# Kernel tuning notes

Hardware: AMD Instinct MI355X
Metric: run time of the kernel (lower is better)

## Reference

```python
import jax, jax.numpy as jnp
import numpy as np

D_MODEL = 512
D_STATE = 64
D_CONV = 4
EXPAND = 2
D_INNER = D_MODEL * EXPAND  # 1024
DT_RANK = 32  # ceil(512/16)
BATCH = 2
SEQLEN = 1024


def setup_inputs() -> dict:
    key = jax.random.key(0)
    ks = jax.random.split(key, 8)
    s = 0.02
    x = jax.random.normal(ks[0], (BATCH, SEQLEN, D_MODEL), dtype=jnp.float32)
    W_in = jax.random.normal(ks[1], (2 * D_INNER, D_MODEL), dtype=jnp.float32) * s
    conv_w = jax.random.normal(ks[2], (D_INNER, 1, D_CONV), dtype=jnp.float32) * s
    conv_b = jnp.zeros((D_INNER,), dtype=jnp.float32)
    W_x = jax.random.normal(ks[3], (DT_RANK + 2 * D_STATE, D_INNER), dtype=jnp.float32) * s
    W_dt = jax.random.normal(ks[4], (D_INNER, DT_RANK), dtype=jnp.float32) * s
    b_dt = jax.random.uniform(ks[5], (D_INNER,), dtype=jnp.float32) * (DT_RANK ** -0.5)
    A_log = jnp.log(jnp.arange(1, D_STATE + 1, dtype=jnp.float32))
    D_param = jnp.ones((D_INNER,), dtype=jnp.float32)
    W_out = jax.random.normal(ks[6], (D_MODEL, D_INNER), dtype=jnp.float32) * s
    return {"x": x, "W_in": W_in, "conv_w": conv_w, "conv_b": conv_b,
            "W_x": W_x, "W_dt": W_dt, "b_dt": b_dt, "A_log": A_log,
            "D_param": D_param, "W_out": W_out}


def _mamba_fwd(x, W_in, conv_w, conv_b, W_x, W_dt, b_dt, A_log, D_param, W_out):
    Bb, L, _ = x.shape
    # input projection -> [B,L,2*d_inner], split into SSM branch and gate
    xz = x @ W_in.T
    xs, z = jnp.split(xz, 2, axis=-1)
    # causal depthwise conv1d (torch pads d_conv-1 both sides then slices [:L])
    xc = jnp.transpose(xs, (0, 2, 1))  # [B, d_inner, L]
    xc = jax.lax.conv_general_dilated(
        xc, conv_w, window_strides=(1,), padding=[(D_CONV - 1, 0)],
        dimension_numbers=('NCH', 'OIH', 'NCH'), feature_group_count=D_INNER)
    xc = xc + conv_b[None, :, None]
    xs = jax.nn.silu(jnp.transpose(xc, (0, 2, 1)))  # [B,L,d_inner]
    # selective parameters
    dbc = xs @ W_x.T  # [B,L,dt_rank+2N]
    dt, Bm, Cm = jnp.split(dbc, [DT_RANK, DT_RANK + D_STATE], axis=-1)
    delta = jax.nn.softplus(dt @ W_dt.T + b_dt)  # [B,L,d_inner]
    A = -jnp.exp(A_log)  # [N]
    dA = jnp.exp(delta[..., None] * A)                 # [B,L,D,N]
    dBx = (delta * xs)[..., None] * Bm[:, :, None, :]  # [B,L,D,N]

    def step(h, inp):
        dA_t, dBx_t, C_t = inp
        h = dA_t * h + dBx_t                 # [B,D,N]
        y_t = jnp.einsum('bdn,bn->bd', h, C_t)
        return h, y_t

    h0 = jnp.zeros((Bb, D_INNER, D_STATE), dtype=x.dtype)
    _, ys = jax.lax.scan(step, h0, (jnp.swapaxes(dA, 0, 1),
                                    jnp.swapaxes(dBx, 0, 1),
                                    jnp.swapaxes(Cm, 0, 1)))
    y = jnp.swapaxes(ys, 0, 1) + D_param * xs  # skip term
    y = y * jax.nn.silu(z)                     # gate
    return y @ W_out.T


def reference(x, W_in, conv_w, conv_b, W_x, W_dt, b_dt, A_log, D_param, W_out):
    return _mamba_fwd(x, W_in, conv_w, conv_b, W_x, W_dt, b_dt, A_log, D_param, W_out)
```

## Files before the change

### kernel.cpp

```cpp
#include <hip/hip_runtime.h>
#include <hip/hip_bf16.h>
#include <math.h>

#define D_STATE 64
#define D_INNER 1024
#define DT_RANK 32
#define BATCH 2
#define SEQLEN 1024
#define MTOT (BATCH * SEQLEN)
#define NCC 64
#define CHT 16

typedef __attribute__((ext_vector_type(8))) short bf16x8;
typedef __attribute__((ext_vector_type(4))) float f32x4;

__device__ __forceinline__ float silu_f(float x) { return x / (1.f + __expf(-x)); }

__global__ __launch_bounds__(256) void cast_bf16_k(
    const float* __restrict__ in, __hip_bfloat16* __restrict__ out, int n)
{
    int i = (blockIdx.x * 256 + threadIdx.x) * 4;
    if (i >= n) return;
    float4 v = *(const float4*)(in + i);
    __hip_bfloat16 o[4] = {__float2bfloat16(v.x), __float2bfloat16(v.y),
                           __float2bfloat16(v.z), __float2bfloat16(v.w)};
    *(short4*)(out + i) = *(const short4*)o;
}

__global__ __launch_bounds__(256) void cast3_k(
    const float* __restrict__ p0, __hip_bfloat16* __restrict__ o0,
    const float* __restrict__ p1, __hip_bfloat16* __restrict__ o1,
    const float* __restrict__ p2, __hip_bfloat16* __restrict__ o2)
{
    int b = blockIdx.x;
    const float* in; __hip_bfloat16* out; int base;
    if (b < 1024)      { in = p0; out = o0; base = b; }
    else if (b < 2048) { in = p1; out = o1; base = b - 1024; }
    else               { in = p2; out = o2; base = b - 2048; }
    int i = (base * 256 + threadIdx.x) * 4;
    float4 v = *(const float4*)(in + i);
    __hip_bfloat16 o[4] = {__float2bfloat16(v.x), __float2bfloat16(v.y),
                           __float2bfloat16(v.z), __float2bfloat16(v.w)};
    *(short4*)(out + i) = *(const short4*)o;
}

template<int BM, int BN>
__global__ __launch_bounds__((BM / 64) * (BN / 64) * 64) void gemm_bf16(
    const __hip_bfloat16* __restrict__ A, const __hip_bfloat16* __restrict__ Bt,
    float* __restrict__ C, int M, int N, int K)
{
    constexpr int NW = (BM / 64) * (BN / 64);
    constexpr int NT = NW * 64;
    constexpr int NWN = BN / 64;
    __shared__ __align__(16) short As[BM][40];
    __shared__ __align__(16) short Bs[BN][40];
    const int tid = threadIdx.x;
    const int m0 = blockIdx.y * BM, n0 = blockIdx.x * BN;
    const int wid = tid >> 6, lane = tid & 63;
    const int wm = wid / NWN, wn = wid % NWN;
    const int lrow = lane & 15, lkg = (lane >> 4) * 8;

    f32x4 acc[4][4] = {};

    for (int k0 = 0; k0 < K; k0 += 32) {
        for (int i = tid * 8; i < BM * 32; i += NT * 8) {
            int r = i >> 5, c = i & 31;
            *(bf16x8*)&As[r][c] =
                *(const bf16x8*)(A + (size_t)(m0 + r) * K + k0 + c);
        }
        for (int i = tid * 8; i < BN * 32; i += NT * 8) {
            int r = i >> 5, c = i & 31;
            bf16x8 v = {};
            if (n0 + r < N)
                v = *(const bf16x8*)(Bt + (size_t)(n0 + r) * K + k0 + c);
            *(bf16x8*)&Bs[r][c] = v;
        }
        __syncthreads();
        bf16x8 af[4], bfr[4];
        #pragma unroll
        for (int mi = 0; mi < 4; ++mi)
            af[mi] = *(const bf16x8*)&As[wm * 64 + mi * 16 + lrow][lkg];
        #pragma unroll
        for (int ni = 0; ni < 4; ++ni)
            bfr[ni] = *(const bf16x8*)&Bs[wn * 64 + ni * 16 + lrow][lkg];
        #pragma unroll
        for (int mi = 0; mi < 4; ++mi)
            #pragma unroll
            for (int ni = 0; ni < 4; ++ni)
                acc[mi][ni] = __builtin_amdgcn_mfma_f32_16x16x32_bf16(
                    af[mi], bfr[ni], acc[mi][ni], 0, 0, 0);
        __syncthreads();
    }

    const int rbase = (lane >> 4) * 4;
    #pragma unroll
    for (int mi = 0; mi < 4; ++mi) {
        #pragma unroll
        for (int ni = 0; ni < 4; ++ni) {
            int col = n0 + wn * 64 + ni * 16 + lrow;
            if (col < N) {
                #pragma unroll
                for (int r = 0; r < 4; ++r) {
                    int row = m0 + wm * 64 + mi * 16 + rbase + r;
                    C[(size_t)row * N + col] = acc[mi][ni][r];
                }
            }
        }
    }
}

template<int MF>
__global__ __launch_bounds__(256) void gemm_bf16_w(
    const __hip_bfloat16* __restrict__ A, const __hip_bfloat16* __restrict__ Bt,
    float* __restrict__ C, int M, int N, int K)
{
    const int tid = threadIdx.x;
    const int wid = tid >> 6, lane = tid & 63;
    const int m0 = blockIdx.y * (64 * MF) + wid * (16 * MF);
    const int n0 = blockIdx.x * 64;
    const int lrow = lane & 15, kg8 = (lane >> 4) * 8;

    f32x4 acc[MF][4] = {};
    #pragma unroll 2
    for (int k0 = 0; k0 < K; k0 += 32) {
        bf16x8 af[MF];
        #pragma unroll
        for (int mi = 0; mi < MF; ++mi)
            af[mi] = *(const bf16x8*)(A + (size_t)(m0 + mi * 16 + lrow) * K + k0 + kg8);
        #pragma unroll
        for (int ni = 0; ni < 4; ++ni) {
            int r = n0 + ni * 16 + lrow;
            bf16x8 bv = {};
            if (r < N) bv = *(const bf16x8*)(Bt + (size_t)r * K + k0 + kg8);
            #pragma unroll
            for (int mi = 0; mi < MF; ++mi)
                acc[mi][ni] = __builtin_amdgcn_mfma_f32_16x16x32_bf16(
                    af[mi], bv, acc[mi][ni], 0, 0, 0);
        }
    }
    const int rbase = (lane >> 4) * 4;
    #pragma unroll
    for (int mi = 0; mi < MF; ++mi) {
        #pragma unroll
        for (int ni = 0; ni < 4; ++ni) {
            int col = n0 + ni * 16 + lrow;
            if (col < N) {
                #pragma unroll
                for (int r = 0; r < 4; ++r)
                    C[(size_t)(m0 + mi * 16 + rbase + r) * N + col] = acc[mi][ni][r];
            }
        }
    }
}

__global__ __launch_bounds__(256) void conv_silu_k(
    const float* __restrict__ xz, const float* __restrict__ cw,
    const float* __restrict__ cb, float* __restrict__ xs,
    __hip_bfloat16* __restrict__ xs_bf)
{
    int e = blockIdx.x * 256 + threadIdx.x;
    int d = (e & 255) * 4;
    int ml = e >> 8;
    int l = ml & (SEQLEN - 1);
    int b = ml >> 10;
    float4 c0 = *(const float4*)(cw + (d + 0) * 4);
    float4 c1 = *(const float4*)(cw + (d + 1) * 4);
    float4 c2 = *(const float4*)(cw + (d + 2) * 4);
    float4 c3 = *(const float4*)(cw + (d + 3) * 4);
    float cwk[4][4] = {{c0.x, c0.y, c0.z, c0.w}, {c1.x, c1.y, c1.z, c1.w},
                       {c2.x, c2.y, c2.z, c2.w}, {c3.x, c3.y, c3.z, c3.w}};
    float4 acc = *(const float4*)(cb + d);
    #pragma unroll
    for (int k = 0; k < 4; ++k) {
        int t = l - 3 + k;
        if (t >= 0) {
            float4 xv = *(const float4*)(xz + (size_t)(b * SEQLEN + t) * 2048 + d);
            acc.x = fmaf(xv.x, cwk[0][k], acc.x);
            acc.y = fmaf(xv.y, cwk[1][k], acc.y);
            acc.z = fmaf(xv.z, cwk[2][k], acc.z);
            acc.w = fmaf(xv.w, cwk[3][k], acc.w);
        }
    }
    float4 v = {silu_f(acc.x), silu_f(acc.y), silu_f(acc.z), silu_f(acc.w)};
    size_t o = (size_t)ml * D_INNER + d;
    *(float4*)(xs + o) = v;
    __hip_bfloat16 ob[4] = {__float2bfloat16(v.x), __float2bfloat16(v.y),
                            __float2bfloat16(v.z), __float2bfloat16(v.w)};
    *(short4*)(xs_bf + o) = *(const short4*)ob;
}

__global__ __launch_bounds__(256) void delta_softplus_k(
    const float* __restrict__ dbc, const float* __restrict__ Wdt,
    const float* __restrict__ bdt, float* __restrict__ delta)
{
    const int tid = threadIdx.x;
    const int mg = blockIdx.x * 8;
    #pragma unroll
    for (int j = 0; j < 4; ++j) {
        const int n = tid + j * 256;
        float w[32];
        const float4* wr = (const float4*)(Wdt + (size_t)n * 32);
        #pragma unroll
        for (int q = 0; q < 8; ++q) {
            float4 v = wr[q];
            w[q * 4 + 0] = v.x; w[q * 4 + 1] = v.y;
            w[q * 4 + 2] = v.z; w[q * 4 + 3] = v.w;
        }
        const float bias = bdt[n];
        #pragma unroll
        for (int m = 0; m < 8; ++m) {
            const float* dt = dbc + (size_t)(mg + m) * 160;
            float acc = bias;
            #pragma unroll
            for (int k = 0; k < 32; ++k) acc = fmaf(dt[k], w[k], acc);
            float sp = (acc > 20.f) ? acc : log1pf(__expf(acc));
            delta[(size_t)(mg + m) * D_INNER + n] = sp;
        }
    }
}


#define SLC_A(H, BB, CC) H = fmaf(a, H, dx * BB); p = fmaf(H, CC, p); a *= E;
#define SL_BODY(H, SD, DD, B0, B1, B2, B3, C0, C1, C2, C3, YL) { \
    SD += DD.x; \
    float E = __expf(-DD.x); \
    float a = __expf(DD.x * wn0); \
    float dx = DD.y; float p = 0.f; \
    SLC_A(H[0], B0.x, C0.x) SLC_A(H[1], B0.y, C0.y) SLC_A(H[2], B0.z, C0.z) SLC_A(H[3], B0.w, C0.w) \
    SLC_A(H[4], B1.x, C1.x) SLC_A(H[5], B1.y, C1.y) SLC_A(H[6], B1.z, C1.z) SLC_A(H[7], B1.w, C1.w) \
    SLC_A(H[8], B2.x, C2.x) SLC_A(H[9], B2.y, C2.y) SLC_A(H[10], B2.z, C2.z) SLC_A(H[11], B2.w, C2.w) \
    SLC_A(H[12], B3.x, C3.x) SLC_A(H[13], B3.y, C3.y) SLC_A(H[14], B3.z, C3.z) SLC_A(H[15], B3.w, C3.w) \
    YL = p; }

__global__ __launch_bounds__(256, 2) void scan_local_k(
    const float* __restrict__ delta, const float* __restrict__ xs,
    const float* __restrict__ dbc, const float* __restrict__ Alog,
    float* __restrict__ S, float* __restrict__ sumd, float* __restrict__ xzbuf)
{
    __shared__ float2 ddxs[2][CHT][64];
    __shared__ float yl[2][4][CHT][64];
    const int tid = threadIdx.x;
    const int pair = blockIdx.x & 31;
    const int dblk = (blockIdx.x >> 5) & 15;
    const int b = blockIdx.x >> 9;
    const int d0 = dblk * 64;
    const int cA = pair, cB = pair + 32;
    const int mA = b * SEQLEN + cA * CHT;
    const int mB = b * SEQLEN + cB * CHT;

    #pragma unroll
    for (int i = tid; i < 2 * CHT * 16; i += 256) {
        int s = i >= CHT * 16;
        int j = i - s * CHT * 16;
        int t = j >> 4, dq = (j & 15) * 4;
        int mbase = s ? mB : mA;
        size_t idx = (size_t)(mbase + t) * D_INNER + d0 + dq;
        float4 dl = *(const float4*)(delta + idx);
        float4 xv = *(const float4*)(xs + idx);
        float4 w1 = {dl.x, dl.x * xv.x, dl.y, dl.y * xv.y};
        float4 w2 = {dl.z, dl.z * xv.z, dl.w, dl.w * xv.w};
        *(float4*)&ddxs[s][t][dq] = w1;
        *(float4*)&ddxs[s][t][dq + 2] = w2;
    }
    __syncthreads();

    const int w = tid >> 6, lane = tid & 63;
    const int nbu = __builtin_amdgcn_readfirstlane(w * 16);
    const float* __restrict__ BpA = dbc + (size_t)mA * 160 + 32 + nbu;
    const float* __restrict__ BpB = dbc + (size_t)mB * 160 + 32 + nbu;
    const float wn0 = -__expf(Alog[nbu]);
    float ha[16], hb[16];
    #pragma unroll
    for (int i = 0; i < 16; ++i) { ha[i] = 0.f; hb[i] = 0.f; }
    float sdA = 0.f, sdB = 0.f;

    #pragma unroll 2
    for (int t = 0; t < CHT; ++t) {
        float2 dA = ddxs[0][t][lane];
        float2 dB = ddxs[1][t][lane];
        float4 A0 = *(const float4*)(BpA + t * 160);
        float4 A1 = *(const float4*)(BpA + t * 160 + 4);
        float4 A2 = *(const float4*)(BpA + t * 160 + 8);
        float4 A3 = *(const float4*)(BpA + t * 160 + 12);
        float4 AC0 = *(const float4*)(BpA + t * 160 + 64);
        float4 AC1 = *(const float4*)(BpA + t * 160 + 68);
        float4 AC2 = *(const float4*)(BpA + t * 160 + 72);
        float4 AC3 = *(const float4*)(BpA + t * 160 + 76);
        float4 B0 = *(const float4*)(BpB + t * 160);
        float4 B1 = *(const float4*)(BpB + t * 160 + 4);
        float4 B2 = *(const float4*)(BpB + t * 160 + 8);
        float4 B3 = *(const float4*)(BpB + t * 160 + 12);
        float4 BC0 = *(const float4*)(BpB + t * 160 + 64);
        float4 BC1 = *(const float4*)(BpB + t * 160 + 68);
        float4 BC2 = *(const float4*)(BpB + t * 160 + 72);
        float4 BC3 = *(const float4*)(BpB + t * 160 + 76);
        SL_BODY(ha, sdA, dA, A0, A1, A2, A3, AC0, AC1, AC2, AC3, yl[0][w][t][lane])
        SL_BODY(hb, sdB, dB, B0, B1, B2, B3, BC0, BC1, BC2, BC3, yl[1][w][t][lane])
    }

    size_t baseA = ((size_t)(b * NCC + cA) * 16 + dblk) * 4096;
    size_t baseB = ((size_t)(b * NCC + cB) * 16 + dblk) * 4096;
    #pragma unroll
    for (int i = 0; i < 16; ++i) {
        S[baseA + (size_t)(nbu + i) * 64 + lane] = ha[i];
        S[baseB + (size_t)(nbu + i) * 64 + lane] = hb[i];
    }
    if (w == 0) {
        sumd[(size_t)(b * NCC + cA) * D_INNER + d0 + lane] = sdA;
        sumd[(size_t)(b * NCC + cB) * D_INNER + d0 + lane] = sdB;
    }
    __syncthreads();

    #pragma unroll
    for (int i = tid; i < 2 * CHT * 16; i += 256) {
        int s = i >= CHT * 16;
        int j = i - s * CHT * 16;
        int t = j >> 4, dq = (j & 15) * 4;
        int m = (s ? mB : mA) + t;
        float4 y0 = *(const float4*)&yl[s][0][t][dq];
        float4 y1 = *(const float4*)&yl[s][1][t][dq];
        float4 y2 = *(const float4*)&yl[s][2][t][dq];
        float4 y3 = *(const float4*)&yl[s][3][t][dq];
        float4 yv = {y0.x + y1.x + y2.x + y3.x, y0.y + y1.y + y2.y + y3.y,
                     y0.z + y1.z + y2.z + y3.z, y0.w + y1.w + y2.w + y3.w};
        *(float4*)(xzbuf + (size_t)m * 2048 + d0 + dq) = yv;
    }
}

__global__ __launch_bounds__(256) void scan_mid_k(
    float* SH, const float* __restrict__ sumd, const float* __restrict__ Alog)
{
    int g = blockIdx.x * 256 + threadIdx.x;
    int d = g & 63;
    int n = (g >> 6) & 63;
    int dblk = (g >> 12) & 15;
    int b = g >> 16;
    float An = -__expf(Alog[n]);
    float h = 0.f;
    #pragma unroll 4
    for (int c = 0; c < NCC; ++c) {
        size_t idx = ((size_t)(b * NCC + c) * 16 + dblk) * 4096 + (size_t)n * 64 + d;
        float s = SH[idx];
        float P = __expf(An * sumd[(size_t)(b * NCC + c) * D_INNER + dblk * 64 + d]);
        SH[idx] = h;
        h = fmaf(P, h, s);
    }
}

#define CR_A(H, CC) p = fmaf(ai * H, CC, p); ai *= E;
#define CR_BODY(H, CD, C0, C1, C2, C3, YL) { \
    float a = __expf(CD * wn0); \
    float E = __expf(-CD); \
    float ai = a; float p = 0.f; \
    CR_A(H[0], C0.x) CR_A(H[1], C0.y) CR_A(H[2], C0.z) CR_A(H[3], C0.w) \
    CR_A(H[4], C1.x) CR_A(H[5], C1.y) CR_A(H[6], C1.z) CR_A(H[7], C1.w) \
    CR_A(H[8], C2.x) CR_A(H[9], C2.y) CR_A(H[10], C2.z) CR_A(H[11], C2.w) \
    CR_A(H[12], C3.x) CR_A(H[13], C3.y) CR_A(H[14], C3.z) CR_A(H[15], C3.w) \
    YL = p; }

__global__ __launch_bounds__(256, 2) void scan_corr_k(
    const float* __restrict__ delta, const float* __restrict__ xs,
    const float* __restrict__ dbc, const float* __restrict__ Alog,
    const float* __restrict__ H, const float* __restrict__ xz,
    const float* __restrict__ Dp, __hip_bfloat16* __restrict__ y)
{
    __shared__ float cum[2][CHT][64];
    __shared__ float yl[2][4][CHT][64];
    const int tid = threadIdx.x;
    const int pair = blockIdx.x & 31;
    const int dblk = (blockIdx.x >> 5) & 15;
    const int b = blockIdx.x >> 9;
    const int d0 = dblk * 64;
    const int cA = pair, cB = pair + 32;
    const int mA = b * SEQLEN + cA * CHT;
    const int mB = b * SEQLEN + cB * CHT;

    #pragma unroll
    for (int i = tid; i < 2 * CHT * 16; i += 256) {
        int s = i >= CHT * 16;
        int j = i - s * CHT * 16;
        int t = j >> 4, dq = (j & 15) * 4;
        int mbase = s ? mB : mA;
        *(float4*)&cum[s][t][dq] =
            *(const float4*)(delta + (size_t)(mbase + t) * D_INNER + d0 + dq);
    }
    __syncthreads();
    if (tid < 128) {
        int s = tid >> 6, d = tid & 63;
        float run = 0.f;
        #pragma unroll
        for (int t = 0; t < CHT; ++t) {
            run += cum[s][t][d];
            cum[s][t][d] = run;
        }
    }
    __syncthreads();

    const int w = tid >> 6, lane = tid & 63;
    const int nbu = __builtin_amdgcn_readfirstlane(w * 16);
    const float* __restrict__ CpA = dbc + (size_t)mA * 160 + 96 + nbu;
    const float* __restrict__ CpB = dbc + (size_t)mB * 160 + 96 + nbu;
    const float wn0 = -__expf(Alog[nbu]);
    size_t baseA = ((size_t)(b * NCC + cA) * 16 + dblk) * 4096;
    size_t baseB = ((size_t)(b * NCC + cB) * 16 + dblk) * 4096;
    float ha[16], hb[16];
    #pragma unroll
    for (int i = 0; i < 16; ++i) {
        ha[i] = H[baseA + (size_t)(nbu + i) * 64 + lane];
        hb[i] = H[baseB + (size_t)(nbu + i) * 64 + lane];
    }

    #pragma unroll 4
    for (int t = 0; t < CHT; ++t) {
        float cdA = cum[0][t][lane];
        float cdB = cum[1][t][lane];
        float4 CA0 = *(const float4*)(CpA + t * 160);
        float4 CA1 = *(const float4*)(CpA + t * 160 + 4);
        float4 CA2 = *(const float4*)(CpA + t * 160 + 8);
        float4 CA3 = *(const float4*)(CpA + t * 160 + 12);
        float4 CB0 = *(const float4*)(CpB + t * 160);
        float4 CB1 = *(const float4*)(CpB + t * 160 + 4);
        float4 CB2 = *(const float4*)(CpB + t * 160 + 8);
        float4 CB3 = *(const float4*)(CpB + t * 160 + 12);
        CR_BODY(ha, cdA, CA0, CA1, CA2, CA3, yl[0][w][t][lane])
        CR_BODY(hb, cdB, CB0, CB1, CB2, CB3, yl[1][w][t][lane])
    }
    __syncthreads();

    #pragma unroll
    for (int i = tid; i < 2 * CHT * 16; i += 256) {
        int s = i >= CHT * 16;
        int j = i - s * CHT * 16;
        int t = j >> 4, dq = (j & 15) * 4;
        int m = (s ? mB : mA) + t;
        int dg = d0 + dq;
        float4 y0 = *(const float4*)&yl[s][0][t][dq];
        float4 y1 = *(const float4*)&yl[s][1][t][dq];
        float4 y2 = *(const float4*)&yl[s][2][t][dq];
        float4 y3 = *(const float4*)&yl[s][3][t][dq];
        float4 yloc = *(const float4*)(xz + (size_t)m * 2048 + dg);
        float4 yv = {yloc.x + y0.x + y1.x + y2.x + y3.x,
                     yloc.y + y0.y + y1.y + y2.y + y3.y,
                     yloc.z + y0.z + y1.z + y2.z + y3.z,
                     yloc.w + y0.w + y1.w + y2.w + y3.w};
        float4 xv = *(const float4*)(xs + (size_t)m * D_INNER + dg);
        float4 zv = *(const float4*)(xz + (size_t)m * 2048 + D_INNER + dg);
        float4 Dv = *(const float4*)(Dp + dg);
        __hip_bfloat16 o[4] = {
            __float2bfloat16((yv.x + Dv.x * xv.x) * silu_f(zv.x)),
            __float2bfloat16((yv.y + Dv.y * xv.y) * silu_f(zv.y)),
            __float2bfloat16((yv.z + Dv.z * xv.z) * silu_f(zv.z)),
            __float2bfloat16((yv.w + Dv.w * xv.w) * silu_f(zv.w))};
        *(short4*)(y + (size_t)m * D_INNER + dg) = *(const short4*)o;
    }
}

extern "C" void kernel_launch(void* const* d_in, const int* in_sizes, int n_in,
                              void* d_out, int out_size, void* d_ws, size_t ws_size,
                              hipStream_t stream)
{
    const float* x    = (const float*)d_in[0];
    const float* Win  = (const float*)d_in[1];
    const float* cw   = (const float*)d_in[2];
    const float* cb   = (const float*)d_in[3];
    const float* Wx   = (const float*)d_in[4];
    const float* Wdt  = (const float*)d_in[5];
    const float* bdt  = (const float*)d_in[6];
    const float* Alog = (const float*)d_in[7];
    const float* Dp   = (const float*)d_in[8];
    const float* Wout = (const float*)d_in[9];
    float* out = (float*)d_out;

    float* ws    = (float*)d_ws;
    float* xz    = ws;
    float* xs    = xz + (size_t)4194304;
    float* dbc   = xs + (size_t)2097152;
    float* delta = dbc + (size_t)327680;
    float* bfreg = delta + (size_t)2097152;
    float* Sbuf  = bfreg + (size_t)2097152;
    float* sumd  = Sbuf + (size_t)2 * NCC * 16 * 4096;
    float* wxbfr = sumd + (size_t)2 * NCC * 1024;

    __hip_bfloat16* bfb     = (__hip_bfloat16*)bfreg;
    __hip_bfloat16* x_bf    = bfb;
    __hip_bfloat16* Win_bf  = bfb + 1048576;
    __hip_bfloat16* xs_bf   = bfb + 2097152;
    __hip_bfloat16* yg_bf   = bfb;
    __hip_bfloat16* Wout_bf = bfb + 2097152;
    __hip_bfloat16* Wx_bf   = (__hip_bfloat16*)wxbfr;

    dim3 blk(256);
    cast3_k<<<dim3(2208), blk, 0, stream>>>(x, x_bf, Win, Win_bf, Wx, Wx_bf);
    gemm_bf16<128, 128><<<dim3(16, 16), blk, 0, stream>>>(
        x_bf, Win_bf, xz, MTOT, 2 * D_INNER, 512);
    conv_silu_k<<<dim3(MTOT * D_INNER / 1024), blk, 0, stream>>>(xz, cw, cb, xs, xs_bf);
    gemm_bf16_w<1><<<dim3(3, 32), blk, 0, stream>>>(xs_bf, Wx_bf, dbc, MTOT, 160, D_INNER);
    delta_softplus_k<<<dim3(MTOT / 8), blk, 0, stream>>>(dbc, Wdt, bdt, delta);
    scan_local_k<<<dim3(BATCH * 16 * 32), blk, 0, stream>>>(
        delta, xs, dbc, Alog, Sbuf, sumd, xz);
    scan_mid_k<<<dim3(512), blk, 0, stream>>>(Sbuf, sumd, Alog);
    scan_corr_k<<<dim3(BATCH * 16 * 32), blk, 0, stream>>>(
        delta, xs, dbc, Alog, Sbuf, xz, Dp, yg_bf);
    cast_bf16_k<<<dim3(512), blk, 0, stream>>>(Wout, Wout_bf, 524288);
    gemm_bf16_w<2><<<dim3(8, 16), blk, 0, stream>>>(yg_bf, Wout_bf, out, MTOT, 512, D_INNER);
}
```

Measured before the change: 192.3 us.

## Fuse delta projection and softplus into local scan, pass cumulative delta to correction

Removes the separate delta_softplus kernel: each scan_local thread computes its own delta from the dt rows and W_dt kept in registers, then writes the running chunk-cumulative delta to a buffer. scan_corr reads that cumulative sum instead of reloading delta and prefix-summing in shared memory. Launch bounds are raised to 4 blocks per SM. The cost is that each of the 4 waves recomputes the same 32-term dot product per delta (redundant ALU), and the higher occupancy target may pressure registers given the 32-float wdt array.

```diff
diff --git a/kernel.cpp b/kernel.cpp
--- a/kernel.cpp
+++ b/kernel.cpp
@@ -189,55 +189,72 @@
     *(short4*)(xs_bf + o) = *(const short4*)ob;
 }
 
-__global__ __launch_bounds__(256) void delta_softplus_k(
-    const float* __restrict__ dbc, const float* __restrict__ Wdt,
-    const float* __restrict__ bdt, float* __restrict__ delta)
-{
-    const int tid = threadIdx.x;
-    const int mg = blockIdx.x * 8;
-    #pragma unroll
-    for (int j = 0; j < 4; ++j) {
-        const int n = tid + j * 256;
-        float w[32];
-        const float4* wr = (const float4*)(Wdt + (size_t)n * 32);
-        #pragma unroll
-        for (int q = 0; q < 8; ++q) {
-            float4 v = wr[q];
-            w[q * 4 + 0] = v.x; w[q * 4 + 1] = v.y;
-            w[q * 4 + 2] = v.z; w[q * 4 + 3] = v.w;
-        }
-        const float bias = bdt[n];
-        #pragma unroll
-        for (int m = 0; m < 8; ++m) {
-            const float* dt = dbc + (size_t)(mg + m) * 160;
-            float acc = bias;
-            #pragma unroll
-            for (int k = 0; k < 32; ++k) acc = fmaf(dt[k], w[k], acc);
-            float sp = (acc > 20.f) ? acc : log1pf(__expf(acc));
-            delta[(size_t)(mg + m) * D_INNER + n] = sp;
-        }
-    }
-}
-
+
+__device__ __forceinline__ float delta_of(
+    const float* __restrict__ row, const float* wdt, float bd)
+{
+    float4 q0 = *(const float4*)(row);
+    float4 q1 = *(const float4*)(row + 4);
+    float4 q2 = *(const float4*)(row + 8);
+    float4 q3 = *(const float4*)(row + 12);
+    float4 q4 = *(const float4*)(row + 16);
+    float4 q5 = *(const float4*)(row + 20);
+    float4 q6 = *(const float4*)(row + 24);
+    float4 q7 = *(const float4*)(row + 28);
+    float s0 = fmaf(q0.x, wdt[0], bd);
+    s0 = fmaf(q0.y, wdt[1], s0); s0 = fmaf(q0.z, wdt[2], s0);
+    s0 = fmaf(q0.w, wdt[3], s0); s0 = fmaf(q1.x, wdt[4], s0);
+    s0 = fmaf(q1.y, wdt[5], s0); s0 = fmaf(q1.z, wdt[6], s0);
+    s0 = fmaf(q1.w, wdt[7], s0);
+    float s1 = q2.x * wdt[8];
+    s1 = fmaf(q2.y, wdt[9], s1); s1 = fmaf(q2.z, wdt[10], s1);
+    s1 = fmaf(q2.w, wdt[11], s1); s1 = fmaf(q3.x, wdt[12], s1);
+    s1 = fmaf(q3.y, wdt[13], s1); s1 = fmaf(q3.z, wdt[14], s1);
+    s1 = fmaf(q3.w, wdt[15], s1);
+    float s2 = q4.x * wdt[16];
+    s2 = fmaf(q4.y, wdt[17], s2); s2 = fmaf(q4.z, wdt[18], s2);
+    s2 = fmaf(q4.w, wdt[19], s2); s2 = fmaf(q5.x, wdt[20], s2);
+    s2 = fmaf(q5.y, wdt[21], s2); s2 = fmaf(q5.z, wdt[22], s2);
+    s2 = fmaf(q5.w, wdt[23], s2);
+    float s3 = q6.x * wdt[24];
+    s3 = fmaf(q6.y, wdt[25], s3); s3 = fmaf(q6.z, wdt[26], s3);
+    s3 = fmaf(q6.w, wdt[27], s3); s3 = fmaf(q7.x, wdt[28], s3);
+    s3 = fmaf(q7.y, wdt[29], s3); s3 = fmaf(q7.z, wdt[30], s3);
+    s3 = fmaf(q7.w, wdt[31], s3);
+    float acc = (s0 + s1) + (s2 + s3);
+    return (acc > 20.f) ? acc : log1pf(__expf(acc));
+}
 
 #define SLC_A(H, BB, CC) H = fmaf(a, H, dx * BB); p = fmaf(H, CC, p); a *= E;
-#define SL_BODY(H, SD, DD, B0, B1, B2, B3, C0, C1, C2, C3, YL) { \
-    SD += DD.x; \
-    float E = __expf(-DD.x); \
-    float a = __expf(DD.x * wn0); \
-    float dx = DD.y; float p = 0.f; \
-    SLC_A(H[0], B0.x, C0.x) SLC_A(H[1], B0.y, C0.y) SLC_A(H[2], B0.z, C0.z) SLC_A(H[3], B0.w, C0.w) \
-    SLC_A(H[4], B1.x, C1.x) SLC_A(H[5], B1.y, C1.y) SLC_A(H[6], B1.z, C1.z) SLC_A(H[7], B1.w, C1.w) \
-    SLC_A(H[8], B2.x, C2.x) SLC_A(H[9], B2.y, C2.y) SLC_A(H[10], B2.z, C2.z) SLC_A(H[11], B2.w, C2.w) \
-    SLC_A(H[12], B3.x, C3.x) SLC_A(H[13], B3.y, C3.y) SLC_A(H[14], B3.z, C3.z) SLC_A(H[15], B3.w, C3.w) \
+#define SL_BODY(H, SP, XV, Bp, Cp, YL) { \
+    float E = __expf(-SP); \
+    float a = __expf(SP * wn0); \
+    float dx = SP * XV; float p = 0.f; \
+    float4 B0 = *(const float4*)(Bp); \
+    float4 B1 = *(const float4*)(Bp + 4); \
+    float4 B2 = *(const float4*)(Bp + 8); \
+    float4 B3 = *(const float4*)(Bp + 12); \
+    float4 C0 = *(const float4*)(Cp); \
+    float4 C1 = *(const float4*)(Cp + 4); \
+    float4 C2 = *(const float4*)(Cp + 8); \
+    float4 C3 = *(const float4*)(Cp + 12); \
+    SLC_A(H[0], B0.x, C0.x) SLC_A(H[1], B0.y, C0.y) \
+    SLC_A(H[2], B0.z, C0.z) SLC_A(H[3], B0.w, C0.w) \
+    SLC_A(H[4], B1.x, C1.x) SLC_A(H[5], B1.y, C1.y) \
+    SLC_A(H[6], B1.z, C1.z) SLC_A(H[7], B1.w, C1.w) \
+    SLC_A(H[8], B2.x, C2.x) SLC_A(H[9], B2.y, C2.y) \
+    SLC_A(H[10], B2.z, C2.z) SLC_A(H[11], B2.w, C2.w) \
+    SLC_A(H[12], B3.x, C3.x) SLC_A(H[13], B3.y, C3.y) \
+    SLC_A(H[14], B3.z, C3.z) SLC_A(H[15], B3.w, C3.w) \
     YL = p; }
 
-__global__ __launch_bounds__(256, 2) void scan_local_k(
-    const float* __restrict__ delta, const float* __restrict__ xs,
-    const float* __restrict__ dbc, const float* __restrict__ Alog,
-    float* __restrict__ S, float* __restrict__ sumd, float* __restrict__ xzbuf)
-{
-    __shared__ float2 ddxs[2][CHT][64];
+__global__ __launch_bounds__(256, 4) void scan_local_k(
+    const float* __restrict__ xs, const float* __restrict__ dbc,
+    const float* __restrict__ Wdt, const float* __restrict__ bdt,
+    const float* __restrict__ Alog, float* __restrict__ S,
+    float* __restrict__ sumd, float* __restrict__ cumbuf,
+    float* __restrict__ xzbuf)
+{
     __shared__ float yl[2][4][CHT][64];
     const int tid = threadIdx.x;
     const int pair = blockIdx.x & 31;
@@ -247,28 +264,24 @@
     const int cA = pair, cB = pair + 32;
     const int mA = b * SEQLEN + cA * CHT;
     const int mB = b * SEQLEN + cB * CHT;
-
-    #pragma unroll
-    for (int i = tid; i < 2 * CHT * 16; i += 256) {
-        int s = i >= CHT * 16;
-        int j = i - s * CHT * 16;
-        int t = j >> 4, dq = (j & 15) * 4;
-        int mbase = s ? mB : mA;
-        size_t idx = (size_t)(mbase + t) * D_INNER + d0 + dq;
-        float4 dl = *(const float4*)(delta + idx);
-        float4 xv = *(const float4*)(xs + idx);
-        float4 w1 = {dl.x, dl.x * xv.x, dl.y, dl.y * xv.y};
-        float4 w2 = {dl.z, dl.z * xv.z, dl.w, dl.w * xv.w};
-        *(float4*)&ddxs[s][t][dq] = w1;
-        *(float4*)&ddxs[s][t][dq + 2] = w2;
-    }
-    __syncthreads();
-
     const int w = tid >> 6, lane = tid & 63;
     const int nbu = __builtin_amdgcn_readfirstlane(w * 16);
-    const float* __restrict__ BpA = dbc + (size_t)mA * 160 + 32 + nbu;
-    const float* __restrict__ BpB = dbc + (size_t)mB * 160 + 32 + nbu;
+    const int dl = d0 + lane;
+
+    float wdt[32];
+    {
+        const float4* wr = (const float4*)(Wdt + (size_t)dl * 32);
+        #pragma unroll
+        for (int q = 0; q < 8; ++q) {
+            float4 v = wr[q];
+            wdt[q * 4 + 0] = v.x; wdt[q * 4 + 1] = v.y;
+            wdt[q * 4 + 2] = v.z; wdt[q * 4 + 3] = v.w;
+        }
+    }
+    const float bd = bdt[dl];
     const float wn0 = -__expf(Alog[nbu]);
+    const float* __restrict__ RpA = dbc + (size_t)mA * 160;
+    const float* __restrict__ RpB = dbc + (size_t)mB * 160;
     float ha[16], hb[16];
     #pragma unroll
     for (int i = 0; i < 16; ++i) { ha[i] = 0.f; hb[i] = 0.f; }
@@ -276,26 +289,19 @@
 
     #pragma unroll 2
     for (int t = 0; t < CHT; ++t) {
-        float2 dA = ddxs[0][t][lane];
-        float2 dB = ddxs[1][t][lane];
-        float4 A0 = *(const float4*)(BpA + t * 160);
-        float4 A1 = *(const float4*)(BpA + t * 160 + 4);
-        float4 A2 = *(const float4*)(BpA + t * 160 + 8);
-        float4 A3 = *(const float4*)(BpA + t * 160 + 12);
-        float4 AC0 = *(const float4*)(BpA + t * 160 + 64);
-        float4 AC1 = *(const float4*)(BpA + t * 160 + 68);
-        float4 AC2 = *(const float4*)(BpA + t * 160 + 72);
-        float4 AC3 = *(const float4*)(BpA + t * 160 + 76);
-        float4 B0 = *(const float4*)(BpB + t * 160);
-        float4 B1 = *(const float4*)(BpB + t * 160 + 4);
-        float4 B2 = *(const float4*)(BpB + t * 160 + 8);
-        float4 B3 = *(const float4*)(BpB + t * 160 + 12);
-        float4 BC0 = *(const float4*)(BpB + t * 160 + 64);
-        float4 BC1 = *(const float4*)(BpB + t * 160 + 68);
-        float4 BC2 = *(const float4*)(BpB + t * 160 + 72);
-        float4 BC3 = *(const float4*)(BpB + t * 160 + 76);
-        SL_BODY(ha, sdA, dA, A0, A1, A2, A3, AC0, AC1, AC2, AC3, yl[0][w][t][lane])
-        SL_BODY(hb, sdB, dB, B0, B1, B2, B3, BC0, BC1, BC2, BC3, yl[1][w][t][lane])
+        const float* rowA = RpA + t * 160;
+        const float* rowB = RpB + t * 160;
+        float spA = delta_of(rowA, wdt, bd);
+        float spB = delta_of(rowB, wdt, bd);
+        float xvA = xs[(size_t)(mA + t) * D_INNER + dl];
+        float xvB = xs[(size_t)(mB + t) * D_INNER + dl];
+        sdA += spA; sdB += spB;
+        if (nbu == 0) {
+            cumbuf[(size_t)(mA + t) * D_INNER + dl] = sdA;
+            cumbuf[(size_t)(mB + t) * D_INNER + dl] = sdB;
+        }
+        SL_BODY(ha, spA, xvA, rowA + 32 + nbu, rowA + 96 + nbu, yl[0][w][t][lane])
+        SL_BODY(hb, spB, xvB, rowB + 32 + nbu, rowB + 96 + nbu, yl[1][w][t][lane])
     }
 
     size_t baseA = ((size_t)(b * NCC + cA) * 16 + dblk) * 4096;
@@ -305,9 +311,9 @@
         S[baseA + (size_t)(nbu + i) * 64 + lane] = ha[i];
         S[baseB + (size_t)(nbu + i) * 64 + lane] = hb[i];
     }
-    if (w == 0) {
-        sumd[(size_t)(b * NCC + cA) * D_INNER + d0 + lane] = sdA;
-        sumd[(size_t)(b * NCC + cB) * D_INNER + d0 + lane] = sdB;
+    if (nbu == 0) {
+        sumd[(size_t)(b * NCC + cA) * D_INNER + dl] = sdA;
+        sumd[(size_t)(b * NCC + cB) * D_INNER + dl] = sdB;
     }
     __syncthreads();
 
@@ -348,23 +354,26 @@
 }
 
 #define CR_A(H, CC) p = fmaf(ai * H, CC, p); ai *= E;
-#define CR_BODY(H, CD, C0, C1, C2, C3, YL) { \
+#define CR_BODY(H, CD, Cp, YL) { \
     float a = __expf(CD * wn0); \
     float E = __expf(-CD); \
     float ai = a; float p = 0.f; \
+    float4 C0 = *(const float4*)(Cp); \
+    float4 C1 = *(const float4*)(Cp + 4); \
+    float4 C2 = *(const float4*)(Cp + 8); \
+    float4 C3 = *(const float4*)(Cp + 12); \
     CR_A(H[0], C0.x) CR_A(H[1], C0.y) CR_A(H[2], C0.z) CR_A(H[3], C0.w) \
     CR_A(H[4], C1.x) CR_A(H[5], C1.y) CR_A(H[6], C1.z) CR_A(H[7], C1.w) \
     CR_A(H[8], C2.x) CR_A(H[9], C2.y) CR_A(H[10], C2.z) CR_A(H[11], C2.w) \
     CR_A(H[12], C3.x) CR_A(H[13], C3.y) CR_A(H[14], C3.z) CR_A(H[15], C3.w) \
     YL = p; }
 
-__global__ __launch_bounds__(256, 2) void scan_corr_k(
-    const float* __restrict__ delta, const float* __restrict__ xs,
-    const float* __restrict__ dbc, const float* __restrict__ Alog,
-    const float* __restrict__ H, const float* __restrict__ xz,
+__global__ __launch_bounds__(256, 4) void scan_corr_k(
+    const float* __restrict__ xs, const float* __restrict__ dbc,
+    const float* __restrict__ Alog, const float* __restrict__ H,
+    const float* __restrict__ cumbuf, const float* __restrict__ xz,
     const float* __restrict__ Dp, __hip_bfloat16* __restrict__ y)
 {
-    __shared__ float cum[2][CHT][64];
     __shared__ float yl[2][4][CHT][64];
     const int tid = threadIdx.x;
     const int pair = blockIdx.x & 31;
@@ -374,30 +383,10 @@
     const int cA = pair, cB = pair + 32;
     const int mA = b * SEQLEN + cA * CHT;
     const int mB = b * SEQLEN + cB * CHT;
-
-    #pragma unroll
-    for (int i = tid; i < 2 * CHT * 16; i += 256) {
-        int s = i >= CHT * 16;
-        int j = i - s * CHT * 16;
-        int t = j >> 4, dq = (j & 15) * 4;
-        int mbase = s ? mB : mA;
-        *(float4*)&cum[s][t][dq] =
-            *(const float4*)(delta + (size_t)(mbase + t) * D_INNER + d0 + dq);
-    }
-    __syncthreads();
-    if (tid < 128) {
-        int s = tid >> 6, d = tid & 63;
-        float run = 0.f;
-        #pragma unroll
-        for (int t = 0; t < CHT; ++t) {
-            run += cum[s][t][d];
-            cum[s][t][d] = run;
-        }
-    }
-    __syncthreads();
-
     const int w = tid >> 6, lane = tid & 63;
     const int nbu = __builtin_amdgcn_readfirstlane(w * 16);
+    const int dl = d0 + lane;
+
     const float* __restrict__ CpA = dbc + (size_t)mA * 160 + 96 + nbu;
     const float* __restrict__ CpB = dbc + (size_t)mB * 160 + 96 + nbu;
     const float wn0 = -__expf(Alog[nbu]);
@@ -412,18 +401,10 @@
 
     #pragma unroll 4
     for (int t = 0; t < CHT; ++t) {
-        float cdA = cum[0][t][lane];
-        float cdB = cum[1][t][lane];
-        float4 CA0 = *(const float4*)(CpA + t * 160);
-        float4 CA1 = *(const float4*)(CpA + t * 160 + 4);
-        float4 CA2 = *(const float4*)(CpA + t * 160 + 8);
-        float4 CA3 = *(const float4*)(CpA + t * 160 + 12);
-        float4 CB0 = *(const float4*)(CpB + t * 160);
-        float4 CB1 = *(const float4*)(CpB + t * 160 + 4);
-        float4 CB2 = *(const float4*)(CpB + t * 160 + 8);
-        float4 CB3 = *(const float4*)(CpB + t * 160 + 12);
-        CR_BODY(ha, cdA, CA0, CA1, CA2, CA3, yl[0][w][t][lane])
-        CR_BODY(hb, cdB, CB0, CB1, CB2, CB3, yl[1][w][t][lane])
+        float cdA = cumbuf[(size_t)(mA + t) * D_INNER + dl];
+        float cdB = cumbuf[(size_t)(mB + t) * D_INNER + dl];
+        CR_BODY(ha, cdA, CpA + t * 160, yl[0][w][t][lane])
+        CR_BODY(hb, cdB, CpB + t * 160, yl[1][w][t][lane])
     }
     __syncthreads();
 
@@ -471,15 +452,15 @@
     const float* Wout = (const float*)d_in[9];
     float* out = (float*)d_out;
 
-    float* ws    = (float*)d_ws;
-    float* xz    = ws;
-    float* xs    = xz + (size_t)4194304;
-    float* dbc   = xs + (size_t)2097152;
-    float* delta = dbc + (size_t)327680;
-    float* bfreg = delta + (size_t)2097152;
-    float* Sbuf  = bfreg + (size_t)2097152;
-    float* sumd  = Sbuf + (size_t)2 * NCC * 16 * 4096;
-    float* wxbfr = sumd + (size_t)2 * NCC * 1024;
+    float* ws     = (float*)d_ws;
+    float* xz     = ws;
+    float* xs     = xz + (size_t)4194304;
+    float* dbc    = xs + (size_t)2097152;
+    float* cumbuf = dbc + (size_t)327680;
+    float* bfreg  = cumbuf + (size_t)2097152;
+    float* Sbuf   = bfreg + (size_t)2097152;
+    float* sumd   = Sbuf + (size_t)2 * NCC * 16 * 4096;
+    float* wxbfr  = sumd + (size_t)2 * NCC * 1024;
 
     __hip_bfloat16* bfb     = (__hip_bfloat16*)bfreg;
     __hip_bfloat16* x_bf    = bfb;
@@ -495,12 +476,11 @@
         x_bf, Win_bf, xz, MTOT, 2 * D_INNER, 512);
     conv_silu_k<<<dim3(MTOT * D_INNER / 1024), blk, 0, stream>>>(xz, cw, cb, xs, xs_bf);
     gemm_bf16_w<1><<<dim3(3, 32), blk, 0, stream>>>(xs_bf, Wx_bf, dbc, MTOT, 160, D_INNER);
-    delta_softplus_k<<<dim3(MTOT / 8), blk, 0, stream>>>(dbc, Wdt, bdt, delta);
     scan_local_k<<<dim3(BATCH * 16 * 32), blk, 0, stream>>>(
-        delta, xs, dbc, Alog, Sbuf, sumd, xz);
+        xs, dbc, Wdt, bdt, Alog, Sbuf, sumd, cumbuf, xz);
     scan_mid_k<<<dim3(512), blk, 0, stream>>>(Sbuf, sumd, Alog);
     scan_corr_k<<<dim3(BATCH * 16 * 32), blk, 0, stream>>>(
-        delta, xs, dbc, Alog, Sbuf, xz, Dp, yg_bf);
+        xs, dbc, Alog, Sbuf, cumbuf, xz, Dp, yg_bf);
     cast_bf16_k<<<dim3(512), blk, 0, stream>>>(Wout, Wout_bf, 524288);
     gemm_bf16_w<2><<<dim3(8, 16), blk, 0, stream>>>(yg_bf, Wout_bf, out, MTOT, 512, D_INNER);
 }
```

Measured after the change: 203.2 us. 1.06x slower.

## Compute delta projection with bf16 MFMA and fold weight casts into one launch

Applied to the files above, without the earlier changes.

The dt-to-delta projection and softplus now run in a dedicated MFMA kernel instead of the earlier scalar delta_softplus kernel. The x_dbl GEMM also writes the dt slice in bf16 to feed it. The W_dt and W_out casts are merged into a single five-way cast launch at the start, which removes the separate W_out cast kernel. This path runs only when the workspace is large enough, and it adds bf16 rounding to the dt rank-32 projection.

```diff
diff --git a/kernel.cpp b/kernel.cpp
--- a/kernel.cpp
+++ b/kernel.cpp
@@ -44,6 +44,27 @@
     *(short4*)(out + i) = *(const short4*)o;
 }
 
+__global__ __launch_bounds__(256) void cast5_k(
+    const float* __restrict__ p0, __hip_bfloat16* __restrict__ o0,
+    const float* __restrict__ p1, __hip_bfloat16* __restrict__ o1,
+    const float* __restrict__ p2, __hip_bfloat16* __restrict__ o2,
+    const float* __restrict__ p3, __hip_bfloat16* __restrict__ o3,
+    const float* __restrict__ p4, __hip_bfloat16* __restrict__ o4)
+{
+    int b = blockIdx.x;
+    const float* in; __hip_bfloat16* out; int base;
+    if (b < 1024)      { in = p0; out = o0; base = b; }
+    else if (b < 2048) { in = p1; out = o1; base = b - 1024; }
+    else if (b < 2208) { in = p2; out = o2; base = b - 2048; }
+    else if (b < 2240) { in = p3; out = o3; base = b - 2208; }
+    else               { in = p4; out = o4; base = b - 2240; }
+    int i = (base * 256 + threadIdx.x) * 4;
+    float4 v = *(const float4*)(in + i);
+    __hip_bfloat16 o[4] = {__float2bfloat16(v.x), __float2bfloat16(v.y),
+                           __float2bfloat16(v.z), __float2bfloat16(v.w)};
+    *(short4*)(out + i) = *(const short4*)o;
+}
+
 template<int BM, int BN>
 __global__ __launch_bounds__((BM / 64) * (BN / 64) * 64) void gemm_bf16(
     const __hip_bfloat16* __restrict__ A, const __hip_bfloat16* __restrict__ Bt,
@@ -109,10 +130,10 @@
     }
 }
 
-template<int MF>
+template<int MF, bool EMIT_DT>
 __global__ __launch_bounds__(256) void gemm_bf16_w(
     const __hip_bfloat16* __restrict__ A, const __hip_bfloat16* __restrict__ Bt,
-    float* __restrict__ C, int M, int N, int K)
+    float* __restrict__ C, int M, int N, int K, __hip_bfloat16* __restrict__ dtbf)
 {
     const int tid = threadIdx.x;
     const int wid = tid >> 6, lane = tid & 63;
@@ -146,8 +167,49 @@
             int col = n0 + ni * 16 + lrow;
             if (col < N) {
                 #pragma unroll
-                for (int r = 0; r < 4; ++r)
-                    C[(size_t)(m0 + mi * 16 + rbase + r) * N + col] = acc[mi][ni][r];
+                for (int r = 0; r < 4; ++r) {
+                    int row = m0 + mi * 16 + rbase + r;
+                    C[(size_t)row * N + col] = acc[mi][ni][r];
+                    if (EMIT_DT && col < DT_RANK)
+                        dtbf[(size_t)row * DT_RANK + col] =
+                            __float2bfloat16(acc[mi][ni][r]);
+                }
+            }
+        }
+    }
+}
+
+__global__ __launch_bounds__(256) void delta_mfma_k(
+    const __hip_bfloat16* __restrict__ dtbf, const __hip_bfloat16* __restrict__ Wdtbf,
+    const float* __restrict__ bdt, float* __restrict__ delta)
+{
+    const int tid = threadIdx.x;
+    const int wid = tid >> 6, lane = tid & 63;
+    const int m0 = blockIdx.y * 128 + wid * 32;
+    const int n0 = blockIdx.x * 64;
+    const int lrow = lane & 15, kg8 = (lane >> 4) * 8;
+
+    f32x4 acc[2][4] = {};
+    bf16x8 af0 = *(const bf16x8*)(dtbf + (size_t)(m0 + lrow) * DT_RANK + kg8);
+    bf16x8 af1 = *(const bf16x8*)(dtbf + (size_t)(m0 + 16 + lrow) * DT_RANK + kg8);
+    #pragma unroll
+    for (int ni = 0; ni < 4; ++ni) {
+        bf16x8 bv = *(const bf16x8*)(Wdtbf + (size_t)(n0 + ni * 16 + lrow) * DT_RANK + kg8);
+        acc[0][ni] = __builtin_amdgcn_mfma_f32_16x16x32_bf16(af0, bv, acc[0][ni], 0, 0, 0);
+        acc[1][ni] = __builtin_amdgcn_mfma_f32_16x16x32_bf16(af1, bv, acc[1][ni], 0, 0, 0);
+    }
+    const int rbase = (lane >> 4) * 4;
+    #pragma unroll
+    for (int mi = 0; mi < 2; ++mi) {
+        #pragma unroll
+        for (int ni = 0; ni < 4; ++ni) {
+            int col = n0 + ni * 16 + lrow;
+            float b = bdt[col];
+            #pragma unroll
+            for (int r = 0; r < 4; ++r) {
+                float a = acc[mi][ni][r] + b;
+                float sp = (a > 20.f) ? a : log1pf(__expf(a));
+                delta[(size_t)(m0 + mi * 16 + rbase + r) * D_INNER + col] = sp;
             }
         }
     }
@@ -480,27 +542,53 @@
     float* Sbuf  = bfreg + (size_t)2097152;
     float* sumd  = Sbuf + (size_t)2 * NCC * 16 * 4096;
     float* wxbfr = sumd + (size_t)2 * NCC * 1024;
+    float* extra = wxbfr + (size_t)81920;
 
     __hip_bfloat16* bfb     = (__hip_bfloat16*)bfreg;
     __hip_bfloat16* x_bf    = bfb;
     __hip_bfloat16* Win_bf  = bfb + 1048576;
     __hip_bfloat16* xs_bf   = bfb + 2097152;
     __hip_bfloat16* yg_bf   = bfb;
-    __hip_bfloat16* Wout_bf = bfb + 2097152;
+    __hip_bfloat16* Wout_bfA = bfb + 2097152;
     __hip_bfloat16* Wx_bf   = (__hip_bfloat16*)wxbfr;
-
+    __hip_bfloat16* Wdt_bf  = (__hip_bfloat16*)extra;
+    __hip_bfloat16* dt_bf   = (__hip_bfloat16*)(extra + 16384);
+    __hip_bfloat16* Wout_bfB = (__hip_bfloat16*)(extra + 49152);
+
+    const bool big = ws_size >= (size_t)19726336 * 4;
     dim3 blk(256);
-    cast3_k<<<dim3(2208), blk, 0, stream>>>(x, x_bf, Win, Win_bf, Wx, Wx_bf);
-    gemm_bf16<128, 128><<<dim3(16, 16), blk, 0, stream>>>(
-        x_bf, Win_bf, xz, MTOT, 2 * D_INNER, 512);
-    conv_silu_k<<<dim3(MTOT * D_INNER / 1024), blk, 0, stream>>>(xz, cw, cb, xs, xs_bf);
-    gemm_bf16_w<1><<<dim3(3, 32), blk, 0, stream>>>(xs_bf, Wx_bf, dbc, MTOT, 160, D_INNER);
-    delta_softplus_k<<<dim3(MTOT / 8), blk, 0, stream>>>(dbc, Wdt, bdt, delta);
-    scan_local_k<<<dim3(BATCH * 16 * 32), blk, 0, stream>>>(
-        delta, xs, dbc, Alog, Sbuf, sumd, xz);
-    scan_mid_k<<<dim3(512), blk, 0, stream>>>(Sbuf, sumd, Alog);
-    scan_corr_k<<<dim3(BATCH * 16 * 32), blk, 0, stream>>>(
-        delta, xs, dbc, Alog, Sbuf, xz, Dp, yg_bf);
-    cast_bf16_k<<<dim3(512), blk, 0, stream>>>(Wout, Wout_bf, 524288);
-    gemm_bf16_w<2><<<dim3(8, 16), blk, 0, stream>>>(yg_bf, Wout_bf, out, MTOT, 512, D_INNER);
-}
+
+    if (big) {
+        cast5_k<<<dim3(2752), blk, 0, stream>>>(
+            x, x_bf, Win, Win_bf, Wx, Wx_bf, Wdt, Wdt_bf, Wout, Wout_bfB);
+        gemm_bf16<128, 128><<<dim3(16, 16), blk, 0, stream>>>(
+            x_bf, Win_bf, xz, MTOT, 2 * D_INNER, 512);
+        conv_silu_k<<<dim3(MTOT * D_INNER / 1024), blk, 0, stream>>>(xz, cw, cb, xs, xs_bf);
+        gemm_bf16_w<1, true><<<dim3(3, 32), blk, 0, stream>>>(
+            xs_bf, Wx_bf, dbc, MTOT, 160, D_INNER, dt_bf);
+        delta_mfma_k<<<dim3(16, 16), blk, 0, stream>>>(dt_bf, Wdt_bf, bdt, delta);
+        scan_local_k<<<dim3(BATCH * 16 * 32), blk, 0, stream>>>(
+            delta, xs, dbc, Alog, Sbuf, sumd, xz);
+        scan_mid_k<<<dim3(512), blk, 0, stream>>>(Sbuf, sumd, Alog);
+        scan_corr_k<<<dim3(BATCH * 16 * 32), blk, 0, stream>>>(
+            delta, xs, dbc, Alog, Sbuf, xz, Dp, yg_bf);
+        gemm_bf16_w<2, false><<<dim3(8, 16), blk, 0, stream>>>(
+            yg_bf, Wout_bfB, out, MTOT, 512, D_INNER, nullptr);
+    } else {
+        cast3_k<<<dim3(2208), blk, 0, stream>>>(x, x_bf, Win, Win_bf, Wx, Wx_bf);
+        gemm_bf16<128, 128><<<dim3(16, 16), blk, 0, stream>>>(
+            x_bf, Win_bf, xz, MTOT, 2 * D_INNER, 512);
+        conv_silu_k<<<dim3(MTOT * D_INNER / 1024), blk, 0, stream>>>(xz, cw, cb, xs, xs_bf);
+        gemm_bf16_w<1, false><<<dim3(3, 32), blk, 0, stream>>>(
+            xs_bf, Wx_bf, dbc, MTOT, 160, D_INNER, nullptr);
+        delta_softplus_k<<<dim3(MTOT / 8), blk, 0, stream>>>(dbc, Wdt, bdt, delta);
+        scan_local_k<<<dim3(BATCH * 16 * 32), blk, 0, stream>>>(
+            delta, xs, dbc, Alog, Sbuf, sumd, xz);
+        scan_mid_k<<<dim3(512), blk, 0, stream>>>(Sbuf, sumd, Alog);
+        scan_corr_k<<<dim3(BATCH * 16 * 32), blk, 0, stream>>>(
+            delta, xs, dbc, Alog, Sbuf, xz, Dp, yg_bf);
+        cast_bf16_k<<<dim3(512), blk, 0, stream>>>(Wout, Wout_bfA, 524288);
+        gemm_bf16_w<2, false><<<dim3(8, 16), blk, 0, stream>>>(
+            yg_bf, Wout_bfA, out, MTOT, 512, D_INNER, nullptr);
+    }
+}
```

Result: faster. 185.6 us (median of 2 runs) (-3.5%).
